# Kernel optimization log

Hardware: AMD Instinct MI355X
Metric: run time of the kernel (lower is better)

Reference implementation:

```python
import jax, jax.numpy as jnp
import numpy as np

B = 65536
CEP_ORDER = 99          # M
IR_LENGTH = 512         # N


def setup_inputs() -> dict:
    key = jax.random.key(0)
    # scale cepstral coeffs like real cepstra (decaying with quefrency) for stability
    scale = 0.5 / (1.0 + jnp.arange(CEP_ORDER + 1, dtype=jnp.float32))
    c = jax.random.normal(key, (B, CEP_ORDER + 1), dtype=jnp.float32) * scale
    return {"c": c}


def reference(c):
    # Oppenheim recursion: h[0] = exp(c[0]); h[n] = (1/n) sum_{m=1}^{min(n,M)} m*c[m]*h[n-m]
    Bc, M1 = c.shape
    M = M1 - 1
    N = IR_LENGTH
    arange = jnp.arange(1, M + 1, dtype=c.dtype)
    c1f = (c[:, 1:] * arange)[:, ::-1]        # flipped weighted cepstrum, [B, M]
    h0 = jnp.exp(c[:, 0])                      # [B]
    # buffer holds h[n-M : n]; zeros for negative indices
    buf0 = jnp.concatenate([jnp.zeros((Bc, M - 1), c.dtype), h0[:, None]], axis=1)

    def step(buf, n):
        hn = jnp.einsum('bm,bm->b', buf, c1f) / n      # [B]
        buf = jnp.concatenate([buf[:, 1:], hn[:, None]], axis=1)
        return buf, hn

    ns = jnp.arange(1, N, dtype=c.dtype)
    _, hs = jax.lax.scan(step, buf0, ns)               # hs: [N-1, B]
    h = jnp.concatenate([h0[:, None], hs.T], axis=1)   # [B, N]
    return h
```

## Files before the change

### kernel.cpp

```cpp
#include <hip/hip_runtime.h>
#include <math.h>


#define NROWS   128
#define STRIDE  129

__device__ __forceinline__ float dpp_xor1(float x) {
    return __int_as_float(__builtin_amdgcn_mov_dpp(__float_as_int(x), 0xB1, 0xF, 0xF, false));
}

__global__ __launch_bounds__(256, 2)
void cep2ir_kernel(const float* __restrict__ c, float* __restrict__ out) {
    __shared__ float stage[NROWS * STRIDE];
    __shared__ float4 rn4[128];
    const int t = threadIdx.x;
    const int lrow = t >> 1;
    const bool isA = (t & 1) == 0;
    const int rowbase = blockIdx.x * NROWS;
    const float* cb = c + (size_t)(rowbase + lrow) * 100;
    float* outb = out + (size_t)rowbase * 512;

    {
        float* rt = reinterpret_cast<float*>(rn4);
        rt[t]       = __builtin_amdgcn_rcpf((float)(t + 1));
        rt[t + 256] = __builtin_amdgcn_rcpf((float)(t + 257));
    }

    float e[52];
    {
        const float4* c4 = reinterpret_cast<const float4*>(cb);
        const int f4b = isA ? 0 : 12;
#pragma unroll
        for (int i = 0; i < 13; ++i) {
            const float4 v = c4[f4b + i];
            e[4 * i + 0] = v.x; e[4 * i + 1] = v.y;
            e[4 * i + 2] = v.z; e[4 * i + 3] = v.w;
        }
    }
    float w[50];
#pragma unroll
    for (int k = 0; k < 49; ++k)
        w[k] = (isA ? e[k + 1] : e[k + 3]) * (isA ? (float)(k + 1) : (float)(k + 51));
    w[49] = isA ? e[50] * 50.0f : 0.0f;

    const float h0 = expf(e[0]);

    float hh[82];
#pragma unroll
    for (int k = 0; k < 82; ++k) hh[k] = 0.0f;
    hh[32] = isA ? h0 : 0.0f;

    if (isA) stage[lrow * STRIDE] = h0;
    __syncthreads();

#pragma unroll 1
    for (int p = 0; p < 4; ++p) {
#pragma unroll 1
        for (int gg = 0; gg < 4; ++gg) {
            float4 r4[8];
            {
                const float4* rp = &rn4[8 * (4 * p + gg)];
#pragma unroll
                for (int i = 0; i < 8; ++i) r4[i] = rp[i];
            }
#pragma unroll
            for (int j = 0; j < 32; ++j) {
                float a0 = 0.f, a1 = 0.f;
#pragma unroll
                for (int k = 49; k >= 0; --k) {
                    if ((k & 1) == 0) a0 = __builtin_fmaf(w[k], hh[k + 32 - j], a0);
                    else              a1 = __builtin_fmaf(w[k], hh[k + 32 - j], a1);
                }
                float s = a0 + a1;
                s += dpp_xor1(s);
                const float rn = (j & 2) ? ((j & 1) ? r4[j >> 2].w : r4[j >> 2].z)
                                         : ((j & 1) ? r4[j >> 2].y : r4[j >> 2].x);
                const float hn = s * rn;
                hh[31 - j] = isA ? hn : hh[31 - j];
            }
            if (isA) {
                float* sc = &stage[lrow * STRIDE + 1 + 32 * gg];
#pragma unroll
                for (int j = 0; j < 32; ++j) sc[j] = hh[31 - j];
            }
            float bv[32];
#pragma unroll
            for (int i = 0; i < 32; ++i) bv[i] = dpp_xor1(hh[18 + i]);
#pragma unroll
            for (int k = 81; k >= 32; --k) hh[k] = hh[k - 32];
#pragma unroll
            for (int i = 0; i < 32; ++i) hh[i] = bv[i];
        }
        __syncthreads();
#pragma unroll 1
        for (int i = 0; i < 64; ++i) {
            const int idx = i * 256 + t;
            const int r = idx >> 7;
            const int cc = idx & 127;
            outb[(size_t)r * 512 + p * 128 + cc] = stage[r * STRIDE + cc];
        }
        __syncthreads();
        if (p < 3 && isA) stage[lrow * STRIDE] = hh[32];
    }
}

extern "C" void kernel_launch(void* const* d_in, const int* in_sizes, int n_in,
                              void* d_out, int out_size, void* d_ws, size_t ws_size,
                              hipStream_t stream) {
    const float* c = (const float*)d_in[0];
    float* out = (float*)d_out;
    cep2ir_kernel<<<512, 256, 0, stream>>>(c, out);
}
```

Baseline: 101.9 us.

## Double-buffer output staging to overlap global stores with recursion compute

Replaces the single 128-column shared staging tile with two 64-column buffers, so each phase computes 64 outputs per row. While one buffer is being filled, the previous phase's buffer is written to global memory, and those stores are interleaved with the next compute groups. This drops one of the two barriers per phase. Stores are also widened to float2. The cost is a different bank pattern from the stride of 66 and a final tail flush after the loop.

```diff
diff --git a/kernel.cpp b/kernel.cpp
--- a/kernel.cpp
+++ b/kernel.cpp
@@ -3,7 +3,7 @@
 
 
 #define NROWS   128
-#define STRIDE  129
+#define STRIDE  66
 
 __device__ __forceinline__ float dpp_xor1(float x) {
     return __int_as_float(__builtin_amdgcn_mov_dpp(__float_as_int(x), 0xB1, 0xF, 0xF, false));
@@ -11,7 +11,7 @@
 
 __global__ __launch_bounds__(256, 2)
 void cep2ir_kernel(const float* __restrict__ c, float* __restrict__ out) {
-    __shared__ float stage[NROWS * STRIDE];
+    __shared__ float buf[2][NROWS * STRIDE];
     __shared__ float4 rn4[128];
     const int t = threadIdx.x;
     const int lrow = t >> 1;
@@ -50,18 +50,32 @@
     for (int k = 0; k < 82; ++k) hh[k] = 0.0f;
     hh[32] = isA ? h0 : 0.0f;
 
-    if (isA) stage[lrow * STRIDE] = h0;
+    if (isA) buf[0][lrow * STRIDE] = h0;
     __syncthreads();
 
 #pragma unroll 1
-    for (int p = 0; p < 4; ++p) {
+    for (int p = 0; p < 8; ++p) {
+        if (p > 0 && isA) buf[p & 1][lrow * STRIDE] = hh[32];
 #pragma unroll 1
-        for (int gg = 0; gg < 4; ++gg) {
+        for (int g = 0; g < 2; ++g) {
+            const int gidx = 2 * p + g;
             float4 r4[8];
             {
-                const float4* rp = &rn4[8 * (4 * p + gg)];
+                const float4* rp = &rn4[8 * gidx];
 #pragma unroll
                 for (int i = 0; i < 8; ++i) r4[i] = rp[i];
+            }
+            if (p > 0) {
+                const float* fb = buf[(p & 1) ^ 1];
+                const int colbase = 64 * (p - 1);
+#pragma unroll
+                for (int i = 0; i < 8; ++i) {
+                    const int idx = (8 * g + i) * 256 + t;
+                    const int r = idx >> 5;
+                    const int c2 = idx & 31;
+                    const float2 v = *reinterpret_cast<const float2*>(&fb[r * STRIDE + 2 * c2]);
+                    *reinterpret_cast<float2*>(&outb[(size_t)r * 512 + colbase + 2 * c2]) = v;
+                }
             }
 #pragma unroll
             for (int j = 0; j < 32; ++j) {
@@ -79,7 +93,7 @@
                 hh[31 - j] = isA ? hn : hh[31 - j];
             }
             if (isA) {
-                float* sc = &stage[lrow * STRIDE + 1 + 32 * gg];
+                float* sc = &buf[p & 1][lrow * STRIDE + 1 + 32 * g];
 #pragma unroll
                 for (int j = 0; j < 32; ++j) sc[j] = hh[31 - j];
             }
@@ -92,15 +106,14 @@
             for (int i = 0; i < 32; ++i) hh[i] = bv[i];
         }
         __syncthreads();
+    }
 #pragma unroll 1
-        for (int i = 0; i < 64; ++i) {
-            const int idx = i * 256 + t;
-            const int r = idx >> 7;
-            const int cc = idx & 127;
-            outb[(size_t)r * 512 + p * 128 + cc] = stage[r * STRIDE + cc];
-        }
-        __syncthreads();
-        if (p < 3 && isA) stage[lrow * STRIDE] = hh[32];
+    for (int i = 0; i < 16; ++i) {
+        const int idx = i * 256 + t;
+        const int r = idx >> 5;
+        const int c2 = idx & 31;
+        const float2 v = *reinterpret_cast<const float2*>(&buf[1][r * STRIDE + 2 * c2]);
+        *reinterpret_cast<float2*>(&outb[(size_t)r * 512 + 448 + 2 * c2]) = v;
     }
 }
 
```

Result: no change. 101.2 us (median of 2 runs) (-0.7%).
